# Performance work log

Hardware: AMD Instinct MI355X
Metric: run time of the kernel (lower is better)

## Reference

```python
import jax, jax.numpy as jnp
import numpy as np

N = 50000      # total nodes in batched graph
E = 800000     # total edges
G = 512        # number of graphs in the batch
NF = 32        # input node feature dim
EF = 16        # edge feature dim
HID = [64, 128, 128, 256]


def _seg_mean(vals, ids, num):
    s = jax.ops.segment_sum(vals, ids, num_segments=num)
    c = jax.ops.segment_sum(jnp.ones((vals.shape[0], 1), vals.dtype), ids, num_segments=num)
    return s / jnp.maximum(c, 1.0)


def setup_inputs() -> dict:
    key = jax.random.key(0)
    ks = list(jax.random.split(key, 64))
    it = iter(ks)

    def nk():
        return next(it)

    inp = {}
    inp["x"] = jax.random.normal(nk(), (N, NF), jnp.float32)
    inp["e"] = jax.random.normal(nk(), (E, EF), jnp.float32)
    inp["src"] = jax.random.randint(nk(), (E,), 0, N)
    inp["dst"] = jax.random.randint(nk(), (E,), 0, N)
    inp["gid"] = jnp.sort(jax.random.randint(nk(), (N,), 0, G))
    fin = NF
    for i, f in enumerate(HID):
        inp[f"Wm{i}"] = jax.random.normal(nk(), (fin + EF, f), jnp.float32) / np.sqrt(fin + EF)
        inp[f"bm{i}"] = jnp.zeros((f,), jnp.float32)
        inp[f"Ws{i}"] = jax.random.normal(nk(), (fin, f), jnp.float32) / np.sqrt(fin)
        inp[f"bs{i}"] = jnp.zeros((f,), jnp.float32)
        inp[f"Wc{i}"] = jax.random.normal(nk(), (f, 1), jnp.float32) / np.sqrt(f)
        inp[f"bc{i}"] = jnp.zeros((1,), jnp.float32)
        fin = f
    return inp


def _molconv(x, e, src, dst, Wm, bm, Ws, bs):
    # gather source node feats, condition on edge feats, per-edge MLP
    m = jax.nn.relu(jnp.concatenate([x[src], e], axis=-1) @ Wm + bm)  # [E, out]
    agg = _seg_mean(m, dst, x.shape[0])                               # scatter-mean to dst
    return jax.nn.relu(agg + x @ Ws + bs)                             # [N, out]


def reference(x, e, src, dst, gid,
              Wm0, bm0, Ws0, bs0, Wc0, bc0,
              Wm1, bm1, Ws1, bs1, Wc1, bc1,
              Wm2, bm2, Ws2, bs2, Wc2, bc2,
              Wm3, bm3, Ws3, bs3, Wc3, bc3):
    layers = [(Wm0, bm0, Ws0, bs0, Wc0, bc0),
              (Wm1, bm1, Ws1, bs1, Wc1, bc1),
              (Wm2, bm2, Ws2, bs2, Wc2, bc2),
              (Wm3, bm3, Ws3, bs3, Wc3, bc3)]
    feat = x
    score = jnp.zeros((G, 1), x.dtype)
    for Wm, bm, Ws, bs, Wc, bc in layers:
        feat = _molconv(feat, e, src, dst, Wm, bm, Ws, bs)
        # per-layer Linear(feats,1) classifier + AvgPooling per graph, summed
        score = score + _seg_mean(feat @ Wc + bc, gid, G)
    return score
```

## Files before the change

### kernel.cpp

```cpp
#include <hip/hip_runtime.h>

#define NN 50000
#define EE 800000
#define GG 512
#define NP 50048
#define EB 3125
#define SCB 196

typedef short bf16x8 __attribute__((ext_vector_type(8)));
typedef float floatx4 __attribute__((ext_vector_type(4)));

__device__ inline unsigned short f2b(float f) {
    unsigned u = __float_as_uint(f);
    unsigned r = (u + 0x7fffu + ((u >> 16) & 1u)) >> 16;
    return (unsigned short)r;
}
__device__ inline float b2f(unsigned short b) {
    return __uint_as_float(((unsigned)b) << 16);
}


__global__ void conv_all(const float* __restrict__ x, unsigned short* __restrict__ xb, long n8x,
                         const float* __restrict__ ef, unsigned short* __restrict__ efB, long n8e) {
    long i = (long)blockIdx.x * blockDim.x + threadIdx.x;
    const float* s;
    unsigned short* d;
    long idx;
    if (i < n8x) { s = x; d = xb; idx = i; }
    else if (i < n8x + n8e) { s = ef; d = efB; idx = i - n8x; }
    else return;
    float4 a = ((const float4*)s)[2 * idx];
    float4 b = ((const float4*)s)[2 * idx + 1];
    unsigned short o[8] = {f2b(a.x), f2b(a.y), f2b(a.z), f2b(a.w),
                           f2b(b.x), f2b(b.y), f2b(b.z), f2b(b.w)};
    ((uint4*)d)[idx] = *(uint4*)o;
}


struct TpD { const float* W; unsigned short* WT; int K, F, Kp, rowOff; };
struct TpTab { TpD d[12]; };

__global__ void tp_all(TpTab t) {
    TpD dd = t.d[blockIdx.y];
    int f = blockIdx.x;
    if (f >= dd.F) return;
    for (int k = threadIdx.x; k < dd.Kp; k += blockDim.x)
        dd.WT[(size_t)f * dd.Kp + k] =
            (k < dd.K) ? f2b(dd.W[(size_t)(dd.rowOff + k) * dd.F + f]) : (unsigned short)0;
}


__global__ void hist_cnt(const int* __restrict__ dst, int* __restrict__ hist,
                         const int* __restrict__ gid, float* __restrict__ gcnt) {
    int b = blockIdx.x;
    if (b < EB) {
        int e = b * 256 + threadIdx.x;
        if (e < EE) atomicAdd(&hist[dst[e]], 1);
    } else {
        int n = (b - EB) * 256 + threadIdx.x;
        if (n < NN) atomicAdd(&gcnt[gid[n]], 1.0f);
    }
}

__global__ void scanA(const int* __restrict__ hist, int* __restrict__ bsum) {
    __shared__ int sb[256];
    int idx = blockIdx.x * 256 + threadIdx.x;
    sb[threadIdx.x] = (idx < NN) ? hist[idx] : 0;
    __syncthreads();
    for (int off = 128; off > 0; off >>= 1) {
        if (threadIdx.x < off) sb[threadIdx.x] += sb[threadIdx.x + off];
        __syncthreads();
    }
    if (threadIdx.x == 0) bsum[blockIdx.x] = sb[0];
}

__global__ void scanB(const int* __restrict__ bsum, int* __restrict__ boff) {
    __shared__ int sb[256];
    int t = threadIdx.x;
    int v = (t < SCB) ? bsum[t] : 0;
    sb[t] = v;
    __syncthreads();
    for (int off = 1; off < 256; off <<= 1) {
        int u = (t >= off) ? sb[t - off] : 0;
        __syncthreads();
        sb[t] += u;
        __syncthreads();
    }
    if (t < SCB) boff[t] = sb[t] - v;
}

__global__ void scanC(const int* __restrict__ hist, const int* __restrict__ boff,
                      int* __restrict__ cursor, float* __restrict__ invdeg,
                      float* __restrict__ gcnt, float* __restrict__ score,
                      const float* __restrict__ bc0, const float* __restrict__ bc1,
                      const float* __restrict__ bc2, const float* __restrict__ bc3) {
    __shared__ int sb[256];
    int t = threadIdx.x;
    int idx = blockIdx.x * 256 + t;
    int v = (idx < NN) ? hist[idx] : 0;
    sb[t] = v;
    __syncthreads();
    for (int off = 1; off < 256; off <<= 1) {
        int u = (t >= off) ? sb[t - off] : 0;
        __syncthreads();
        sb[t] += u;
        __syncthreads();
    }
    if (idx < NN) {
        cursor[idx] = boff[blockIdx.x] + sb[t] - v;
        invdeg[idx] = 1.0f / fmaxf((float)v, 1.0f);
    }
    if (idx < GG) {
        float c = gcnt[idx];
        gcnt[idx] = 1.0f / fmaxf(c, 1.0f);
        score[idx] = (c > 0.0f) ? (bc0[0] + bc1[0] + bc2[0] + bc3[0]) : 0.0f;
    }
}

__global__ void scatter_kernel(const int* __restrict__ src, const int* __restrict__ dst,
                               int* __restrict__ cursor, const unsigned short* __restrict__ efB,
                               int* __restrict__ srcS, int* __restrict__ dstS,
                               unsigned short* __restrict__ efS) {
    int e = blockIdx.x * blockDim.x + threadIdx.x;
    if (e < EE) {
        int d = dst[e];
        int p = atomicAdd(&cursor[d], 1);
        srcS[p] = src[e];
        dstS[p] = d;
        const uint4* s = (const uint4*)&efB[(size_t)e * 16];
        uint4* dd = (uint4*)&efS[(size_t)p * 16];
        dd[0] = s[0];
        dd[1] = s[1];
    }
}


template<int FIN, int F>
__global__ __launch_bounds__(256)
void nodeP(const unsigned short* __restrict__ featB, const unsigned short* __restrict__ WxT,
           unsigned short* __restrict__ P)
{
    const int tid = threadIdx.x;
    const int w   = tid >> 6;
    const int l   = tid & 63;
    const int l16 = l & 15;
    const int q   = l >> 4;
    const int cb  = blockIdx.y * 64;
    const int nb  = blockIdx.x * 64;
    const int row = nb + w * 16 + l16;

    floatx4 acc[4];
    #pragma unroll
    for (int nt = 0; nt < 4; ++nt) acc[nt] = (floatx4){0.f, 0.f, 0.f, 0.f};

    #pragma unroll
    for (int kb = 0; kb < FIN; kb += 32) {
        bf16x8 a = *(const bf16x8*)&featB[(size_t)row * FIN + kb + q * 8];
        #pragma unroll
        for (int nt = 0; nt < 4; ++nt) {
            bf16x8 b = *(const bf16x8*)&WxT[(size_t)(cb + nt * 16 + l16) * FIN + kb + q * 8];
            acc[nt] = __builtin_amdgcn_mfma_f32_16x16x32_bf16(a, b, acc[nt], 0, 0, 0);
        }
    }

    #pragma unroll
    for (int nt = 0; nt < 4; ++nt)
        #pragma unroll
        for (int r = 0; r < 4; ++r) {
            int ro = nb + w * 16 + q * 4 + r;
            P[(size_t)ro * F + cb + nt * 16 + l16] = f2b(acc[nt][r]);
        }
}


template<int F>
__global__ __launch_bounds__(256)
void edge_q(const unsigned short* __restrict__ efS,
            const int* __restrict__ srcS, const int* __restrict__ dstS,
            const unsigned short* __restrict__ WeT, const unsigned short* __restrict__ P,
            const float* __restrict__ bm, float* __restrict__ agg)
{
    constexpr int CW  = (F >= 128) ? 128 : 64;
    constexpr int WPG = F / CW;
    constexpr int NT  = CW / 16;
    constexpr int EPB = 64 * (4 / WPG);
    constexpr int RS  = (CW == 128) ? 132 : 68;

    __shared__ __align__(16) float red[4][16 * RS];

    const int tid = threadIdx.x;
    const int w   = tid >> 6;
    const int l   = tid & 63;
    const int l16 = l & 15;
    const int q   = l >> 4;
    const int sub = w / WPG;
    const int cb  = (w % WPG) * CW;
    const int be  = blockIdx.x * EPB + sub * 64;

    const int dreg = dstS[be + l];
    const int sreg = srcS[be + l];

    const bf16x8 ZV = {0, 0, 0, 0, 0, 0, 0, 0};

    bf16x8 bfr[NT];
    #pragma unroll
    for (int nt = 0; nt < NT; ++nt)
        bfr[nt] = *(const bf16x8*)&WeT[(size_t)(cb + nt * 16 + l16) * 32 + q * 8];

    if constexpr (CW == 128) {
        float2 bmv;
        bmv.x = bm[cb + 2 * l];
        bmv.y = bm[cb + 2 * l + 1];

        int cur_d = -1;
        float2 csum = {0.f, 0.f};
        bool from_start = false;

        #pragma unroll
        for (int mt = 0; mt < 4; ++mt) {
            bf16x8 a = ZV;
            if (q < 2) a = *(const bf16x8*)&efS[(size_t)(be + mt * 16 + l16) * 16 + q * 8];
            floatx4 acc[NT];
            #pragma unroll
            for (int nt = 0; nt < NT; ++nt)
                acc[nt] = __builtin_amdgcn_mfma_f32_16x16x32_bf16(
                    a, bfr[nt], (floatx4){0.f, 0.f, 0.f, 0.f}, 0, 0, 0);

            unsigned pvv[16];
            #pragma unroll
            for (int r = 0; r < 16; ++r) {
                int sr = __shfl(sreg, mt * 16 + r);
                pvv[r] = *(const unsigned*)&P[(size_t)sr * F + cb + 2 * l];
            }

            #pragma unroll
            for (int nt = 0; nt < NT; ++nt)
                #pragma unroll
                for (int r4 = 0; r4 < 4; ++r4)
                    red[w][(q * 4 + r4) * RS + nt * 16 + l16] = acc[nt][r4];

            #pragma unroll
            for (int r = 0; r < 16; ++r) {
                int gr = mt * 16 + r;
                int d = __shfl(dreg, gr);
                float2 qv = *(const float2*)&red[w][r * RS + 2 * l];
                float2 v;
                v.x = fmaxf(qv.x + __uint_as_float(pvv[r] << 16)         + bmv.x, 0.f);
                v.y = fmaxf(qv.y + __uint_as_float(pvv[r] & 0xffff0000u) + bmv.y, 0.f);
                if (gr == 0) {
                    cur_d = d; csum = v; from_start = true;
                } else if (d != cur_d) {
                    float* ap = &agg[(size_t)cur_d * F + cb + 2 * l];
                    if (from_start) { atomicAdd(ap, csum.x); atomicAdd(ap + 1, csum.y); }
                    else            { *(float2*)ap = csum; }
                    cur_d = d; csum = v; from_start = false;
                } else {
                    csum.x += v.x; csum.y += v.y;
                }
            }
        }
        float* ap = &agg[(size_t)cur_d * F + cb + 2 * l];
        atomicAdd(ap, csum.x);
        atomicAdd(ap + 1, csum.y);
    } else {
        const float bmv = bm[cb + l];

        int cur_d = -1;
        float csum = 0.f;
        bool from_start = false;

        #pragma unroll
        for (int mt = 0; mt < 4; ++mt) {
            bf16x8 a = ZV;
            if (q < 2) a = *(const bf16x8*)&efS[(size_t)(be + mt * 16 + l16) * 16 + q * 8];
            floatx4 acc[NT];
            #pragma unroll
            for (int nt = 0; nt < NT; ++nt)
                acc[nt] = __builtin_amdgcn_mfma_f32_16x16x32_bf16(
                    a, bfr[nt], (floatx4){0.f, 0.f, 0.f, 0.f}, 0, 0, 0);

            float pv[16];
            #pragma unroll
            for (int r = 0; r < 16; ++r) {
                int sr = __shfl(sreg, mt * 16 + r);
                pv[r] = b2f(P[(size_t)sr * F + cb + l]);
            }

            #pragma unroll
            for (int nt = 0; nt < NT; ++nt)
                #pragma unroll
                for (int r4 = 0; r4 < 4; ++r4)
                    red[w][(q * 4 + r4) * RS + nt * 16 + l16] = acc[nt][r4];

            #pragma unroll
            for (int r = 0; r < 16; ++r) {
                int gr = mt * 16 + r;
                int d = __shfl(dreg, gr);
                float v = fmaxf(red[w][r * RS + l] + pv[r] + bmv, 0.f);
                if (gr == 0) {
                    cur_d = d; csum = v; from_start = true;
                } else if (d != cur_d) {
                    float* ap = &agg[(size_t)cur_d * F + cb + l];
                    if (from_start) atomicAdd(ap, csum);
                    else *ap = csum;
                    cur_d = d; csum = v; from_start = false;
                } else {
                    csum += v;
                }
            }
        }
        atomicAdd(&agg[(size_t)cur_d * F + cb + l], csum);
    }
}


template<int FIN, int F>
__global__ __launch_bounds__(256)
void node_mfma(const unsigned short* __restrict__ featB, const float* __restrict__ agg,
               const unsigned short* __restrict__ WsT, const float* __restrict__ bs,
               const float* __restrict__ Wc, const float* __restrict__ invdeg,
               unsigned short* __restrict__ fout, float* __restrict__ rd)
{
    const int tid = threadIdx.x;
    const int w   = tid >> 6;
    const int l   = tid & 63;
    const int l16 = l & 15;
    const int q   = l >> 4;
    const int cb  = blockIdx.y * 64;
    const int nb  = blockIdx.x * 64;
    const int row = nb + w * 16 + l16;

    floatx4 acc[4];
    #pragma unroll
    for (int nt = 0; nt < 4; ++nt) acc[nt] = (floatx4){0.f, 0.f, 0.f, 0.f};

    #pragma unroll
    for (int kb = 0; kb < FIN; kb += 32) {
        bf16x8 a = *(const bf16x8*)&featB[(size_t)row * FIN + kb + q * 8];
        #pragma unroll
        for (int nt = 0; nt < 4; ++nt) {
            bf16x8 b = *(const bf16x8*)&WsT[(size_t)(cb + nt * 16 + l16) * FIN + kb + q * 8];
            acc[nt] = __builtin_amdgcn_mfma_f32_16x16x32_bf16(a, b, acc[nt], 0, 0, 0);
        }
    }

    float wcv[4], bsv[4];
    #pragma unroll
    for (int nt = 0; nt < 4; ++nt) {
        wcv[nt] = Wc[cb + nt * 16 + l16];
        bsv[nt] = bs[cb + nt * 16 + l16];
    }

    #pragma unroll
    for (int r = 0; r < 4; ++r) {
        int n = nb + w * 16 + q * 4 + r;
        bool valid = n < NN;
        float idg = valid ? invdeg[n] : 0.f;
        float s = 0.f;
        #pragma unroll
        for (int nt = 0; nt < 4; ++nt) {
            int col = cb + nt * 16 + l16;
            float av = valid ? agg[(size_t)n * F + col] : 0.f;
            float v = fmaxf(acc[nt][r] + av * idg + bsv[nt], 0.f);
            if (valid) fout[(size_t)n * F + col] = f2b(v);
            s += v * wcv[nt];
        }
        s += __shfl_xor(s, 1);
        s += __shfl_xor(s, 2);
        s += __shfl_xor(s, 4);
        s += __shfl_xor(s, 8);
        if (valid && l16 == 0) atomicAdd(&rd[n], s);
    }
}


__global__ void score_reduce(const float* __restrict__ rd, const int* __restrict__ gid,
                             const float* __restrict__ invg, float* __restrict__ score) {
    int n = blockIdx.x * blockDim.x + threadIdx.x;
    int l = threadIdx.x & 63;
    bool valid = n < NN;
    int g = valid ? gid[n] : -1;
    float v = valid ? rd[n] : 0.f;
    #pragma unroll
    for (int off = 1; off < 64; off <<= 1) {
        float vo = __shfl_up(v, off);
        int go = __shfl_up(g, off);
        if (l >= off && go == g) v += vo;
    }
    int gn = __shfl_down(g, 1);
    bool tail = (l == 63) || (gn != g);
    if (valid && tail) atomicAdd(&score[g], v * invg[g]);
}


extern "C" void kernel_launch(void* const* d_in, const int* in_sizes, int n_in,
                              void* d_out, int out_size, void* d_ws, size_t ws_size,
                              hipStream_t stream) {
    const float* x   = (const float*)d_in[0];
    const float* ef  = (const float*)d_in[1];
    const int*   src = (const int*)d_in[2];
    const int*   dst = (const int*)d_in[3];
    const int*   gid = (const int*)d_in[4];
    const float *Wm[4], *bm[4], *Ws[4], *bs[4], *Wc[4], *bc[4];
    for (int i = 0; i < 4; ++i) {
        Wm[i] = (const float*)d_in[5 + 6 * i];
        bm[i] = (const float*)d_in[6 + 6 * i];
        Ws[i] = (const float*)d_in[7 + 6 * i];
        bs[i] = (const float*)d_in[8 + 6 * i];
        Wc[i] = (const float*)d_in[9 + 6 * i];
        bc[i] = (const float*)d_in[10 + 6 * i];
    }

    char* w = (char*)d_ws;
    float* agg = (float*)w;                  w += (size_t)NN * 256 * 4;
    unsigned short* xb  = (unsigned short*)w; w += (size_t)NP * 32 * 2;
    unsigned short* f1  = (unsigned short*)w; w += (size_t)NP * 64 * 2;
    unsigned short* f2  = (unsigned short*)w; w += (size_t)NP * 128 * 2;
    unsigned short* f3  = (unsigned short*)w; w += (size_t)NP * 128 * 2;
    unsigned short* f4  = (unsigned short*)w; w += (size_t)NP * 256 * 2;
    unsigned short* P   = (unsigned short*)w; w += (size_t)NP * 256 * 2;
    unsigned short* efB = (unsigned short*)w; w += (size_t)EE * 16 * 2;
    unsigned short* efS = (unsigned short*)w; w += (size_t)EE * 16 * 2;
    unsigned short* WxT0 = (unsigned short*)w; w += (size_t)64 * 32 * 2;
    unsigned short* WxT1 = (unsigned short*)w; w += (size_t)128 * 64 * 2;
    unsigned short* WxT2 = (unsigned short*)w; w += (size_t)128 * 128 * 2;
    unsigned short* WxT3 = (unsigned short*)w; w += (size_t)256 * 128 * 2;
    unsigned short* WeT0 = (unsigned short*)w; w += (size_t)64 * 32 * 2;
    unsigned short* WeT1 = (unsigned short*)w; w += (size_t)128 * 32 * 2;
    unsigned short* WeT2 = (unsigned short*)w; w += (size_t)128 * 32 * 2;
    unsigned short* WeT3 = (unsigned short*)w; w += (size_t)256 * 32 * 2;
    unsigned short* WsT0 = (unsigned short*)w; w += (size_t)64 * 32 * 2;
    unsigned short* WsT1 = (unsigned short*)w; w += (size_t)128 * 64 * 2;
    unsigned short* WsT2 = (unsigned short*)w; w += (size_t)128 * 128 * 2;
    unsigned short* WsT3 = (unsigned short*)w; w += (size_t)256 * 128 * 2;
    float* invdeg = (float*)w;               w += (size_t)NN * 4;
    float* invg   = (float*)w;               w += (size_t)GG * 4;
    float* rd     = (float*)w;               w += (size_t)NN * 4;
    int* hist   = (int*)w;                   w += (size_t)(NN + 1) * 4;
    int* srcS   = (int*)w;                   w += (size_t)EE * 4;
    int* dstS   = (int*)w;                   w += (size_t)EE * 4;
    int* bsum   = (int*)w;                   w += (size_t)SCB * 4;
    int* boff   = (int*)w;                   w += (size_t)SCB * 4;
    int* cursor = (int*)w;                   w += (size_t)NN * 4;
    float* score = (float*)d_out;

    const long n8x = (long)NN * 32 / 8, n8e = (long)EE * 16 / 8;
    conv_all<<<(n8x + n8e + 255) / 256, 256, 0, stream>>>(x, xb, n8x, ef, efB, n8e);

    TpTab tt;
    tt.d[0]  = {Wm[0], WxT0,  32,  64,  32,   0};
    tt.d[1]  = {Wm[1], WxT1,  64, 128,  64,   0};
    tt.d[2]  = {Wm[2], WxT2, 128, 128, 128,   0};
    tt.d[3]  = {Wm[3], WxT3, 128, 256, 128,   0};
    tt.d[4]  = {Wm[0], WeT0,  16,  64,  32,  32};
    tt.d[5]  = {Wm[1], WeT1,  16, 128,  32,  64};
    tt.d[6]  = {Wm[2], WeT2,  16, 128,  32, 128};
    tt.d[7]  = {Wm[3], WeT3,  16, 256,  32, 128};
    tt.d[8]  = {Ws[0], WsT0,  32,  64,  32,   0};
    tt.d[9]  = {Ws[1], WsT1,  64, 128,  64,   0};
    tt.d[10] = {Ws[2], WsT2, 128, 128, 128,   0};
    tt.d[11] = {Ws[3], WsT3, 128, 256, 128,   0};
    tp_all<<<dim3(256, 12), 256, 0, stream>>>(tt);

    hipMemsetAsync(invg, 0, (size_t)(GG + NN + NN + 1) * 4, stream);
    hist_cnt<<<EB + SCB, 256, 0, stream>>>(dst, hist, gid, invg);
    scanA<<<SCB, 256, 0, stream>>>(hist, bsum);
    scanB<<<1, 256, 0, stream>>>(bsum, boff);
    scanC<<<SCB, 256, 0, stream>>>(hist, boff, cursor, invdeg, invg, score,
                                   bc[0], bc[1], bc[2], bc[3]);
    scatter_kernel<<<EB, 256, 0, stream>>>(src, dst, cursor, efB, srcS, dstS, efS);

    const int NB = NP / 64;

    nodeP<32, 64><<<dim3(NB, 1), 256, 0, stream>>>(xb, WxT0, P);
    hipMemsetAsync(agg, 0, (size_t)NN * 64 * 4, stream);
    edge_q<64><<<EB, 256, 0, stream>>>(efS, srcS, dstS, WeT0, P, bm[0], agg);
    node_mfma<32, 64><<<dim3(NB, 1), 256, 0, stream>>>(xb, agg, WsT0, bs[0], Wc[0], invdeg, f1, rd);

    nodeP<64, 128><<<dim3(NB, 2), 256, 0, stream>>>(f1, WxT1, P);
    hipMemsetAsync(agg, 0, (size_t)NN * 128 * 4, stream);
    edge_q<128><<<EB, 256, 0, stream>>>(efS, srcS, dstS, WeT1, P, bm[1], agg);
    node_mfma<64, 128><<<dim3(NB, 2), 256, 0, stream>>>(f1, agg, WsT1, bs[1], Wc[1], invdeg, f2, rd);

    nodeP<128, 128><<<dim3(NB, 2), 256, 0, stream>>>(f2, WxT2, P);
    hipMemsetAsync(agg, 0, (size_t)NN * 128 * 4, stream);
    edge_q<128><<<EB, 256, 0, stream>>>(efS, srcS, dstS, WeT2, P, bm[2], agg);
    node_mfma<128, 128><<<dim3(NB, 2), 256, 0, stream>>>(f2, agg, WsT2, bs[2], Wc[2], invdeg, f3, rd);

    nodeP<128, 256><<<dim3(NB, 4), 256, 0, stream>>>(f3, WxT3, P);
    hipMemsetAsync(agg, 0, (size_t)NN * 256 * 4, stream);
    edge_q<256><<<EE / 128, 256, 0, stream>>>(efS, srcS, dstS, WeT3, P, bm[3], agg);
    node_mfma<128, 256><<<dim3(NB, 4), 256, 0, stream>>>(f3, agg, WsT3, bs[3], Wc[3], invdeg, f4, rd);

    score_reduce<<<SCB, 256, 0, stream>>>(rd, gid, invg, score);
}
```

Measured before the change: 710.9 us.

## Fuse agg zeroing into nodeP, prefetch edge tiles, swizzle LDS staging

The aggregation buffer is now zeroed inside the nodeP kernel instead of by a separate memset per layer, which saves a launch and one pass over memory. In edge_q, the edge-feature fragment and the gathered P values for the next 16-edge tile are loaded while the current tile is processed, so gather latency overlaps with compute. The LDS staging buffer drops its row padding and uses an XOR swizzle instead to avoid bank conflicts. In exchange, the double-buffered arrays raise register pressure.

```diff
diff --git a/kernel.cpp b/kernel.cpp
--- a/kernel.cpp
+++ b/kernel.cpp
@@ -138,7 +138,7 @@
 template<int FIN, int F>
 __global__ __launch_bounds__(256)
 void nodeP(const unsigned short* __restrict__ featB, const unsigned short* __restrict__ WxT,
-           unsigned short* __restrict__ P)
+           unsigned short* __restrict__ P, float* __restrict__ agg)
 {
     const int tid = threadIdx.x;
     const int w   = tid >> 6;
@@ -148,6 +148,17 @@
     const int cb  = blockIdx.y * 64;
     const int nb  = blockIdx.x * 64;
     const int row = nb + w * 16 + l16;
+
+    {
+        const int zr = nb + (tid >> 4);
+        const int zc = cb + ((tid & 15) << 2);
+        const float4 z4 = {0.f, 0.f, 0.f, 0.f};
+        #pragma unroll
+        for (int i = 0; i < 4; ++i) {
+            int n = zr + i * 16;
+            if (n < NN) *(float4*)&agg[(size_t)n * F + zc] = z4;
+        }
+    }
 
     floatx4 acc[4];
     #pragma unroll
@@ -184,7 +195,7 @@
     constexpr int WPG = F / CW;
     constexpr int NT  = CW / 16;
     constexpr int EPB = 64 * (4 / WPG);
-    constexpr int RS  = (CW == 128) ? 132 : 68;
+    constexpr int RS  = CW;
 
     __shared__ __align__(16) float red[4][16 * RS];
 
@@ -201,6 +212,8 @@
     const int sreg = srcS[be + l];
 
     const bf16x8 ZV = {0, 0, 0, 0, 0, 0, 0, 0};
+    const int xo = q << 3;
+    float* redw = &red[w][0];
 
     bf16x8 bfr[NT];
     #pragma unroll
@@ -216,36 +229,43 @@
         float2 csum = {0.f, 0.f};
         bool from_start = false;
 
+        bf16x8 a_cur = ZV, a_nxt;
+        if (q < 2) a_cur = *(const bf16x8*)&efS[(size_t)(be + l16) * 16 + q * 8];
+        unsigned pvv[16], pvn[16];
+        #pragma unroll
+        for (int r = 0; r < 16; ++r) {
+            int sr = __shfl(sreg, r);
+            pvv[r] = *(const unsigned*)&P[(size_t)sr * F + cb + 2 * l];
+        }
+
         #pragma unroll
         for (int mt = 0; mt < 4; ++mt) {
-            bf16x8 a = ZV;
-            if (q < 2) a = *(const bf16x8*)&efS[(size_t)(be + mt * 16 + l16) * 16 + q * 8];
-            floatx4 acc[NT];
+            if (mt < 3) {
+                a_nxt = ZV;
+                if (q < 2) a_nxt = *(const bf16x8*)&efS[(size_t)(be + (mt + 1) * 16 + l16) * 16 + q * 8];
+            }
             #pragma unroll
-            for (int nt = 0; nt < NT; ++nt)
-                acc[nt] = __builtin_amdgcn_mfma_f32_16x16x32_bf16(
-                    a, bfr[nt], (floatx4){0.f, 0.f, 0.f, 0.f}, 0, 0, 0);
-
-            unsigned pvv[16];
-            #pragma unroll
-            for (int r = 0; r < 16; ++r) {
-                int sr = __shfl(sreg, mt * 16 + r);
-                pvv[r] = *(const unsigned*)&P[(size_t)sr * F + cb + 2 * l];
-            }
-
-            #pragma unroll
-            for (int nt = 0; nt < NT; ++nt)
+            for (int nt = 0; nt < NT; ++nt) {
+                floatx4 acc = __builtin_amdgcn_mfma_f32_16x16x32_bf16(
+                    a_cur, bfr[nt], (floatx4){0.f, 0.f, 0.f, 0.f}, 0, 0, 0);
                 #pragma unroll
                 for (int r4 = 0; r4 < 4; ++r4)
-                    red[w][(q * 4 + r4) * RS + nt * 16 + l16] = acc[nt][r4];
-
+                    redw[(q * 4 + r4) * RS + ((nt * 16 + l16) ^ xo)] = acc[r4];
+            }
+            if (mt < 3) {
+                #pragma unroll
+                for (int r = 0; r < 16; ++r) {
+                    int sr = __shfl(sreg, (mt + 1) * 16 + r);
+                    pvn[r] = *(const unsigned*)&P[(size_t)sr * F + cb + 2 * l];
+                }
+            }
             #pragma unroll
             for (int r = 0; r < 16; ++r) {
                 int gr = mt * 16 + r;
                 int d = __shfl(dreg, gr);
-                float2 qv = *(const float2*)&red[w][r * RS + 2 * l];
+                float2 qv = *(const float2*)&redw[r * RS + ((2 * l) ^ (((r >> 2) & 3) << 3))];
                 float2 v;
-                v.x = fmaxf(qv.x + __uint_as_float(pvv[r] << 16)         + bmv.x, 0.f);
+                v.x = fmaxf(qv.x + __uint_as_float(pvv[r] << 16)          + bmv.x, 0.f);
                 v.y = fmaxf(qv.y + __uint_as_float(pvv[r] & 0xffff0000u) + bmv.y, 0.f);
                 if (gr == 0) {
                     cur_d = d; csum = v; from_start = true;
@@ -258,6 +278,11 @@
                     csum.x += v.x; csum.y += v.y;
                 }
             }
+            if (mt < 3) {
+                #pragma unroll
+                for (int r = 0; r < 16; ++r) pvv[r] = pvn[r];
+                a_cur = a_nxt;
+            }
         }
         float* ap = &agg[(size_t)cur_d * F + cb + 2 * l];
         atomicAdd(ap, csum.x);
@@ -269,34 +294,42 @@
         float csum = 0.f;
         bool from_start = false;
 
+        bf16x8 a_cur = ZV, a_nxt;
+        if (q < 2) a_cur = *(const bf16x8*)&efS[(size_t)(be + l16) * 16 + q * 8];
+        float pvv[16], pvn[16];
+        #pragma unroll
+        for (int r = 0; r < 16; ++r) {
+            int sr = __shfl(sreg, r);
+            pvv[r] = b2f(P[(size_t)sr * F + cb + l]);
+        }
+
         #pragma unroll
         for (int mt = 0; mt < 4; ++mt) {
-            bf16x8 a = ZV;
-            if (q < 2) a = *(const bf16x8*)&efS[(size_t)(be + mt * 16 + l16) * 16 + q * 8];
-            floatx4 acc[NT];
+            if (mt < 3) {
+                a_nxt = ZV;
+                if (q < 2) a_nxt = *(const bf16x8*)&efS[(size_t)(be + (mt + 1) * 16 + l16) * 16 + q * 8];
+            }
             #pragma unroll
-            for (int nt = 0; nt < NT; ++nt)
-                acc[nt] = __builtin_amdgcn_mfma_f32_16x16x32_bf16(
-                    a, bfr[nt], (floatx4){0.f, 0.f, 0.f, 0.f}, 0, 0, 0);
-
-            float pv[16];
-            #pragma unroll
-            for (int r = 0; r < 16; ++r) {
-                int sr = __shfl(sreg, mt * 16 + r);
-                pv[r] = b2f(P[(size_t)sr * F + cb + l]);
-            }
-
-            #pragma unroll
-            for (int nt = 0; nt < NT; ++nt)
+            for (int nt = 0; nt < NT; ++nt) {
+                floatx4 acc = __builtin_amdgcn_mfma_f32_16x16x32_bf16(
+                    a_cur, bfr[nt], (floatx4){0.f, 0.f, 0.f, 0.f}, 0, 0, 0);
                 #pragma unroll
                 for (int r4 = 0; r4 < 4; ++r4)
-                    red[w][(q * 4 + r4) * RS + nt * 16 + l16] = acc[nt][r4];
-
+                    redw[(q * 4 + r4) * RS + ((nt * 16 + l16) ^ xo)] = acc[r4];
+            }
+            if (mt < 3) {
+                #pragma unroll
+                for (int r = 0; r < 16; ++r) {
+                    int sr = __shfl(sreg, (mt + 1) * 16 + r);
+                    pvn[r] = b2f(P[(size_t)sr * F + cb + l]);
+                }
+            }
             #pragma unroll
             for (int r = 0; r < 16; ++r) {
                 int gr = mt * 16 + r;
                 int d = __shfl(dreg, gr);
-                float v = fmaxf(red[w][r * RS + l] + pv[r] + bmv, 0.f);
+                float qv = redw[r * RS + (l ^ (((r >> 2) & 3) << 3))];
+                float v = fmaxf(qv + pvv[r] + bmv, 0.f);
                 if (gr == 0) {
                     cur_d = d; csum = v; from_start = true;
                 } else if (d != cur_d) {
@@ -307,6 +340,11 @@
                 } else {
                     csum += v;
                 }
+            }
+            if (mt < 3) {
+                #pragma unroll
+                for (int r = 0; r < 16; ++r) pvv[r] = pvn[r];
+                a_cur = a_nxt;
             }
         }
         atomicAdd(&agg[(size_t)cur_d * F + cb + l], csum);
@@ -472,23 +510,19 @@
 
     const int NB = NP / 64;
 
-    nodeP<32, 64><<<dim3(NB, 1), 256, 0, stream>>>(xb, WxT0, P);
-    hipMemsetAsync(agg, 0, (size_t)NN * 64 * 4, stream);
+    nodeP<32, 64><<<dim3(NB, 1), 256, 0, stream>>>(xb, WxT0, P, agg);
     edge_q<64><<<EB, 256, 0, stream>>>(efS, srcS, dstS, WeT0, P, bm[0], agg);
     node_mfma<32, 64><<<dim3(NB, 1), 256, 0, stream>>>(xb, agg, WsT0, bs[0], Wc[0], invdeg, f1, rd);
 
-    nodeP<64, 128><<<dim3(NB, 2), 256, 0, stream>>>(f1, WxT1, P);
-    hipMemsetAsync(agg, 0, (size_t)NN * 128 * 4, stream);
+    nodeP<64, 128><<<dim3(NB, 2), 256, 0, stream>>>(f1, WxT1, P, agg);
     edge_q<128><<<EB, 256, 0, stream>>>(efS, srcS, dstS, WeT1, P, bm[1], agg);
     node_mfma<64, 128><<<dim3(NB, 2), 256, 0, stream>>>(f1, agg, WsT1, bs[1], Wc[1], invdeg, f2, rd);
 
-    nodeP<128, 128><<<dim3(NB, 2), 256, 0, stream>>>(f2, WxT2, P);
-    hipMemsetAsync(agg, 0, (size_t)NN * 128 * 4, stream);
+    nodeP<128, 128><<<dim3(NB, 2), 256, 0, stream>>>(f2, WxT2, P, agg);
     edge_q<128><<<EB, 256, 0, stream>>>(efS, srcS, dstS, WeT2, P, bm[2], agg);
     node_mfma<128, 128><<<dim3(NB, 2), 256, 0, stream>>>(f2, agg, WsT2, bs[2], Wc[2], invdeg, f3, rd);
 
-    nodeP<128, 256><<<dim3(NB, 4), 256, 0, stream>>>(f3, WxT3, P);
-    hipMemsetAsync(agg, 0, (size_t)NN * 256 * 4, stream);
+    nodeP<128, 256><<<dim3(NB, 4), 256, 0, stream>>>(f3, WxT3, P, agg);
     edge_q<256><<<EE / 128, 256, 0, stream>>>(efS, srcS, dstS, WeT3, P, bm[3], agg);
     node_mfma<128, 256><<<dim3(NB, 4), 256, 0, stream>>>(f3, agg, WsT3, bs[3], Wc[3], invdeg, f4, rd);
 
```

New measurement: 686.4 us. 3.4% less time.

## Double-buffer edge gathers into LDS, fuse agg zeroing into nodeP

Applied to the files above, without the earlier changes.

The edge kernel now gathers source-node projections and edge features straight into per-wave LDS buffers with asynchronous global-to-LDS loads. It double-buffers them so the next 16-edge tile loads while the current one computes. The column width per wave is fixed at 64 for every layer, so wider layers use more blocks. LDS writes use XOR swizzling to avoid bank conflicts. The separate memset of the aggregation buffer is folded into the nodeP kernel, which removes extra launches and a full write pass, at the cost of hand-written waitcnt bookkeeping.

```diff
diff --git a/kernel.cpp b/kernel.cpp
--- a/kernel.cpp
+++ b/kernel.cpp
@@ -18,6 +18,13 @@
 __device__ inline float b2f(unsigned short b) {
     return __uint_as_float(((unsigned)b) << 16);
 }
+
+#define GLD16(gp, lp) __builtin_amdgcn_global_load_lds( \
+    (const __attribute__((address_space(1))) void*)(gp), \
+    (__attribute__((address_space(3))) void*)(lp), 16, 0, 0)
+#define GLD4(gp, lp) __builtin_amdgcn_global_load_lds( \
+    (const __attribute__((address_space(1))) void*)(gp), \
+    (__attribute__((address_space(3))) void*)(lp), 4, 0, 0)
 
 
 __global__ void conv_all(const float* __restrict__ x, unsigned short* __restrict__ xb, long n8x,
@@ -138,7 +145,7 @@
 template<int FIN, int F>
 __global__ __launch_bounds__(256)
 void nodeP(const unsigned short* __restrict__ featB, const unsigned short* __restrict__ WxT,
-           unsigned short* __restrict__ P)
+           unsigned short* __restrict__ P, float* __restrict__ agg)
 {
     const int tid = threadIdx.x;
     const int w   = tid >> 6;
@@ -149,6 +156,17 @@
     const int nb  = blockIdx.x * 64;
     const int row = nb + w * 16 + l16;
 
+    {
+        const int zr = nb + (tid >> 4);
+        const int zc = cb + ((tid & 15) << 2);
+        const float4 z4 = {0.f, 0.f, 0.f, 0.f};
+        #pragma unroll
+        for (int i = 0; i < 4; ++i) {
+            int n = zr + i * 16;
+            if (n < NN) *(float4*)&agg[(size_t)n * F + zc] = z4;
+        }
+    }
+
     floatx4 acc[4];
     #pragma unroll
     for (int nt = 0; nt < 4; ++nt) acc[nt] = (floatx4){0.f, 0.f, 0.f, 0.f};
@@ -172,6 +190,8 @@
         }
 }
 
+
+#define RXO(r) ((((r) >> 2 & 1) << 4) | (((r) >> 3 & 1) << 3))
 
 template<int F>
 __global__ __launch_bounds__(256)
@@ -180,13 +200,15 @@
             const unsigned short* __restrict__ WeT, const unsigned short* __restrict__ P,
             const float* __restrict__ bm, float* __restrict__ agg)
 {
-    constexpr int CW  = (F >= 128) ? 128 : 64;
+    constexpr int CW  = 64;
     constexpr int WPG = F / CW;
-    constexpr int NT  = CW / 16;
+    constexpr int NT  = 4;
     constexpr int EPB = 64 * (4 / WPG);
-    constexpr int RS  = (CW == 128) ? 132 : 68;
+    constexpr int RS  = 64;
 
     __shared__ __align__(16) float red[4][16 * RS];
+    __shared__ __align__(16) unsigned short stgP[4][2][16 * 64];
+    __shared__ __align__(16) unsigned short stgE[4][2][16 * 16];
 
     const int tid = threadIdx.x;
     const int w   = tid >> 6;
@@ -200,117 +222,82 @@
     const int dreg = dstS[be + l];
     const int sreg = srcS[be + l];
 
+    const int grow = l >> 3;
+    const int gchk = l & 7;
+
     const bf16x8 ZV = {0, 0, 0, 0, 0, 0, 0, 0};
+    const int xo = ((q & 1) << 4) | ((q >> 1) << 3);
+    float* redw = &red[w][0];
 
     bf16x8 bfr[NT];
     #pragma unroll
     for (int nt = 0; nt < NT; ++nt)
         bfr[nt] = *(const bf16x8*)&WeT[(size_t)(cb + nt * 16 + l16) * 32 + q * 8];
 
-    if constexpr (CW == 128) {
-        float2 bmv;
-        bmv.x = bm[cb + 2 * l];
-        bmv.y = bm[cb + 2 * l + 1];
-
-        int cur_d = -1;
-        float2 csum = {0.f, 0.f};
-        bool from_start = false;
-
-        #pragma unroll
-        for (int mt = 0; mt < 4; ++mt) {
-            bf16x8 a = ZV;
-            if (q < 2) a = *(const bf16x8*)&efS[(size_t)(be + mt * 16 + l16) * 16 + q * 8];
-            floatx4 acc[NT];
+    const float bmv = bm[cb + l];
+
+    {
+        int sr0 = __shfl(sreg, grow);
+        int sr1 = __shfl(sreg, 8 + grow);
+        GLD16(&P[(size_t)sr0 * F + cb + gchk * 8], &stgP[w][0][0]);
+        GLD16(&P[(size_t)sr1 * F + cb + gchk * 8], &stgP[w][0][512]);
+        GLD4(&efS[(size_t)(be + grow) * 16 + gchk * 2],      &stgE[w][0][0]);
+        GLD4(&efS[(size_t)(be + 8 + grow) * 16 + gchk * 2],  &stgE[w][0][128]);
+    }
+
+    int cur_d = -1;
+    float csum = 0.f;
+    bool from_start = false;
+
+    #pragma unroll
+    for (int mt = 0; mt < 4; ++mt) {
+        const int bufc = mt & 1;
+        if (mt < 3) {
+            int sr0 = __shfl(sreg, (mt + 1) * 16 + grow);
+            int sr1 = __shfl(sreg, (mt + 1) * 16 + 8 + grow);
+            GLD16(&P[(size_t)sr0 * F + cb + gchk * 8], &stgP[w][bufc ^ 1][0]);
+            GLD16(&P[(size_t)sr1 * F + cb + gchk * 8], &stgP[w][bufc ^ 1][512]);
+            GLD4(&efS[(size_t)(be + (mt + 1) * 16 + grow) * 16 + gchk * 2],
+                 &stgE[w][bufc ^ 1][0]);
+            GLD4(&efS[(size_t)(be + (mt + 1) * 16 + 8 + grow) * 16 + gchk * 2],
+                 &stgE[w][bufc ^ 1][128]);
+        }
+        if (mt < 3) asm volatile("s_waitcnt vmcnt(4)" ::: "memory");
+        else        asm volatile("s_waitcnt vmcnt(0)" ::: "memory");
+        __builtin_amdgcn_sched_barrier(0);
+
+        bf16x8 a = ZV;
+        if (q < 2) a = *(const bf16x8*)&stgE[w][bufc][l16 * 16 + q * 8];
+
+        #pragma unroll
+        for (int nt = 0; nt < NT; ++nt) {
+            floatx4 acc = __builtin_amdgcn_mfma_f32_16x16x32_bf16(
+                a, bfr[nt], (floatx4){0.f, 0.f, 0.f, 0.f}, 0, 0, 0);
             #pragma unroll
-            for (int nt = 0; nt < NT; ++nt)
-                acc[nt] = __builtin_amdgcn_mfma_f32_16x16x32_bf16(
-                    a, bfr[nt], (floatx4){0.f, 0.f, 0.f, 0.f}, 0, 0, 0);
-
-            unsigned pvv[16];
-            #pragma unroll
-            for (int r = 0; r < 16; ++r) {
-                int sr = __shfl(sreg, mt * 16 + r);
-                pvv[r] = *(const unsigned*)&P[(size_t)sr * F + cb + 2 * l];
+            for (int r4 = 0; r4 < 4; ++r4)
+                redw[(q * 4 + r4) * RS + ((nt * 16 + l16) ^ xo)] = acc[r4];
+        }
+
+        const unsigned short* stw = &stgP[w][bufc][0];
+        #pragma unroll
+        for (int r = 0; r < 16; ++r) {
+            int gr = mt * 16 + r;
+            int d = __shfl(dreg, gr);
+            float qv = redw[r * RS + (l ^ RXO(r))];
+            float v = fmaxf(qv + b2f(stw[r * 64 + l]) + bmv, 0.f);
+            if (gr == 0) {
+                cur_d = d; csum = v; from_start = true;
+            } else if (d != cur_d) {
+                float* ap = &agg[(size_t)cur_d * F + cb + l];
+                if (from_start) atomicAdd(ap, csum);
+                else *ap = csum;
+                cur_d = d; csum = v; from_start = false;
+            } else {
+                csum += v;
             }
-
-            #pragma unroll
-            for (int nt = 0; nt < NT; ++nt)
-                #pragma unroll
-                for (int r4 = 0; r4 < 4; ++r4)
-                    red[w][(q * 4 + r4) * RS + nt * 16 + l16] = acc[nt][r4];
-
-            #pragma unroll
-            for (int r = 0; r < 16; ++r) {
-                int gr = mt * 16 + r;
-                int d = __shfl(dreg, gr);
-                float2 qv = *(const float2*)&red[w][r * RS + 2 * l];
-                float2 v;
-                v.x = fmaxf(qv.x + __uint_as_float(pvv[r] << 16)         + bmv.x, 0.f);
-                v.y = fmaxf(qv.y + __uint_as_float(pvv[r] & 0xffff0000u) + bmv.y, 0.f);
-                if (gr == 0) {
-                    cur_d = d; csum = v; from_start = true;
-                } else if (d != cur_d) {
-                    float* ap = &agg[(size_t)cur_d * F + cb + 2 * l];
-                    if (from_start) { atomicAdd(ap, csum.x); atomicAdd(ap + 1, csum.y); }
-                    else            { *(float2*)ap = csum; }
-                    cur_d = d; csum = v; from_start = false;
-                } else {
-                    csum.x += v.x; csum.y += v.y;
-                }
-            }
-        }
-        float* ap = &agg[(size_t)cur_d * F + cb + 2 * l];
-        atomicAdd(ap, csum.x);
-        atomicAdd(ap + 1, csum.y);
-    } else {
-        const float bmv = bm[cb + l];
-
-        int cur_d = -1;
-        float csum = 0.f;
-        bool from_start = false;
-
-        #pragma unroll
-        for (int mt = 0; mt < 4; ++mt) {
-            bf16x8 a = ZV;
-            if (q < 2) a = *(const bf16x8*)&efS[(size_t)(be + mt * 16 + l16) * 16 + q * 8];
-            floatx4 acc[NT];
-            #pragma unroll
-            for (int nt = 0; nt < NT; ++nt)
-                acc[nt] = __builtin_amdgcn_mfma_f32_16x16x32_bf16(
-                    a, bfr[nt], (floatx4){0.f, 0.f, 0.f, 0.f}, 0, 0, 0);
-
-            float pv[16];
-            #pragma unroll
-            for (int r = 0; r < 16; ++r) {
-                int sr = __shfl(sreg, mt * 16 + r);
-                pv[r] = b2f(P[(size_t)sr * F + cb + l]);
-            }
-
-            #pragma unroll
-            for (int nt = 0; nt < NT; ++nt)
-                #pragma unroll
-                for (int r4 = 0; r4 < 4; ++r4)
-                    red[w][(q * 4 + r4) * RS + nt * 16 + l16] = acc[nt][r4];
-
-            #pragma unroll
-            for (int r = 0; r < 16; ++r) {
-                int gr = mt * 16 + r;
-                int d = __shfl(dreg, gr);
-                float v = fmaxf(red[w][r * RS + l] + pv[r] + bmv, 0.f);
-                if (gr == 0) {
-                    cur_d = d; csum = v; from_start = true;
-                } else if (d != cur_d) {
-                    float* ap = &agg[(size_t)cur_d * F + cb + l];
-                    if (from_start) atomicAdd(ap, csum);
-                    else *ap = csum;
-                    cur_d = d; csum = v; from_start = false;
-                } else {
-                    csum += v;
-                }
-            }
-        }
-        atomicAdd(&agg[(size_t)cur_d * F + cb + l], csum);
-    }
+        }
+    }
+    atomicAdd(&agg[(size_t)cur_d * F + cb + l], csum);
 }
 
 
@@ -472,24 +459,20 @@
 
     const int NB = NP / 64;
 
-    nodeP<32, 64><<<dim3(NB, 1), 256, 0, stream>>>(xb, WxT0, P);
-    hipMemsetAsync(agg, 0, (size_t)NN * 64 * 4, stream);
+    nodeP<32, 64><<<dim3(NB, 1), 256, 0, stream>>>(xb, WxT0, P, agg);
     edge_q<64><<<EB, 256, 0, stream>>>(efS, srcS, dstS, WeT0, P, bm[0], agg);
     node_mfma<32, 64><<<dim3(NB, 1), 256, 0, stream>>>(xb, agg, WsT0, bs[0], Wc[0], invdeg, f1, rd);
 
-    nodeP<64, 128><<<dim3(NB, 2), 256, 0, stream>>>(f1, WxT1, P);
-    hipMemsetAsync(agg, 0, (size_t)NN * 128 * 4, stream);
-    edge_q<128><<<EB, 256, 0, stream>>>(efS, srcS, dstS, WeT1, P, bm[1], agg);
+    nodeP<64, 128><<<dim3(NB, 2), 256, 0, stream>>>(f1, WxT1, P, agg);
+    edge_q<128><<<EE / 128, 256, 0, stream>>>(efS, srcS, dstS, WeT1, P, bm[1], agg);
     node_mfma<64, 128><<<dim3(NB, 2), 256, 0, stream>>>(f1, agg, WsT1, bs[1], Wc[1], invdeg, f2, rd);
 
-    nodeP<128, 128><<<dim3(NB, 2), 256, 0, stream>>>(f2, WxT2, P);
-    hipMemsetAsync(agg, 0, (size_t)NN * 128 * 4, stream);
-    edge_q<128><<<EB, 256, 0, stream>>>(efS, srcS, dstS, WeT2, P, bm[2], agg);
+    nodeP<128, 128><<<dim3(NB, 2), 256, 0, stream>>>(f2, WxT2, P, agg);
+    edge_q<128><<<EE / 128, 256, 0, stream>>>(efS, srcS, dstS, WeT2, P, bm[2], agg);
     node_mfma<128, 128><<<dim3(NB, 2), 256, 0, stream>>>(f2, agg, WsT2, bs[2], Wc[2], invdeg, f3, rd);
 
-    nodeP<128, 256><<<dim3(NB, 4), 256, 0, stream>>>(f3, WxT3, P);
-    hipMemsetAsync(agg, 0, (size_t)NN * 256 * 4, stream);
-    edge_q<256><<<EE / 128, 256, 0, stream>>>(efS, srcS, dstS, WeT3, P, bm[3], agg);
+    nodeP<128, 256><<<dim3(NB, 4), 256, 0, stream>>>(f3, WxT3, P, agg);
+    edge_q<256><<<EE / 64, 256, 0, stream>>>(efS, srcS, dstS, WeT3, P, bm[3], agg);
     node_mfma<128, 256><<<dim3(NB, 4), 256, 0, stream>>>(f3, agg, WsT3, bs[3], Wc[3], invdeg, f4, rd);
 
     score_reduce<<<SCB, 256, 0, stream>>>(rd, gid, invg, score);
```

After: 749.3 us. 5.4% more time.

## Fuse agg zeroing into nodeP, ballot segment ends, XOR-swizzle LDS reduction

Applied to the files above, without the earlier changes.

Zeroes the aggregation buffer inside the nodeP kernel, so the four separate memset launches go away. In edge_q, segment boundaries are precomputed with a wave ballot over neighbouring dst values, which replaces the per-row cur_d compare/shuffle chain. The LDS staging buffer drops its padding and uses an XOR swizzle to avoid bank conflicts. MFMA results are now produced and stored per tile, which cuts live accumulator registers. The risk is that the swizzle and boundary logic (first/last segment atomics) must exactly match the old semantics.

```diff
diff --git a/kernel.cpp b/kernel.cpp
--- a/kernel.cpp
+++ b/kernel.cpp
@@ -138,7 +138,7 @@
 template<int FIN, int F>
 __global__ __launch_bounds__(256)
 void nodeP(const unsigned short* __restrict__ featB, const unsigned short* __restrict__ WxT,
-           unsigned short* __restrict__ P)
+           unsigned short* __restrict__ P, float* __restrict__ agg)
 {
     const int tid = threadIdx.x;
     const int w   = tid >> 6;
@@ -149,6 +149,17 @@
     const int nb  = blockIdx.x * 64;
     const int row = nb + w * 16 + l16;
 
+    {
+        const int zr = nb + (tid >> 4);
+        const int zc = cb + ((tid & 15) << 2);
+        const float4 z4 = {0.f, 0.f, 0.f, 0.f};
+        #pragma unroll
+        for (int i = 0; i < 4; ++i) {
+            int n = zr + i * 16;
+            if (n < NN) *(float4*)&agg[(size_t)n * F + zc] = z4;
+        }
+    }
+
     floatx4 acc[4];
     #pragma unroll
     for (int nt = 0; nt < 4; ++nt) acc[nt] = (floatx4){0.f, 0.f, 0.f, 0.f};
@@ -172,6 +183,8 @@
         }
 }
 
+
+#define RXO(r) ((((r) >> 2 & 1) << 4) | (((r) >> 3 & 1) << 3))
 
 template<int F>
 __global__ __launch_bounds__(256)
@@ -184,7 +197,7 @@
     constexpr int WPG = F / CW;
     constexpr int NT  = CW / 16;
     constexpr int EPB = 64 * (4 / WPG);
-    constexpr int RS  = (CW == 128) ? 132 : 68;
+    constexpr int RS  = CW;
 
     __shared__ __align__(16) float red[4][16 * RS];
 
@@ -200,7 +213,12 @@
     const int dreg = dstS[be + l];
     const int sreg = srcS[be + l];
 
+    const int dnext = __shfl_down(dreg, 1);
+    const unsigned long long em = __ballot((l == 63) || (dreg != dnext));
+
     const bf16x8 ZV = {0, 0, 0, 0, 0, 0, 0, 0};
+    const int xo = ((q & 1) << 4) | ((q >> 1) << 3);
+    float* redw = &red[w][0];
 
     bf16x8 bfr[NT];
     #pragma unroll
@@ -212,20 +230,13 @@
         bmv.x = bm[cb + 2 * l];
         bmv.y = bm[cb + 2 * l + 1];
 
-        int cur_d = -1;
         float2 csum = {0.f, 0.f};
-        bool from_start = false;
+        bool first = true;
 
         #pragma unroll
         for (int mt = 0; mt < 4; ++mt) {
             bf16x8 a = ZV;
             if (q < 2) a = *(const bf16x8*)&efS[(size_t)(be + mt * 16 + l16) * 16 + q * 8];
-            floatx4 acc[NT];
-            #pragma unroll
-            for (int nt = 0; nt < NT; ++nt)
-                acc[nt] = __builtin_amdgcn_mfma_f32_16x16x32_bf16(
-                    a, bfr[nt], (floatx4){0.f, 0.f, 0.f, 0.f}, 0, 0, 0);
-
             unsigned pvv[16];
             #pragma unroll
             for (int r = 0; r < 16; ++r) {
@@ -234,82 +245,71 @@
             }
 
             #pragma unroll
-            for (int nt = 0; nt < NT; ++nt)
+            for (int nt = 0; nt < NT; ++nt) {
+                floatx4 acc = __builtin_amdgcn_mfma_f32_16x16x32_bf16(
+                    a, bfr[nt], (floatx4){0.f, 0.f, 0.f, 0.f}, 0, 0, 0);
                 #pragma unroll
                 for (int r4 = 0; r4 < 4; ++r4)
-                    red[w][(q * 4 + r4) * RS + nt * 16 + l16] = acc[nt][r4];
+                    redw[(q * 4 + r4) * RS + ((nt * 16 + l16) ^ xo)] = acc[r4];
+            }
 
             #pragma unroll
             for (int r = 0; r < 16; ++r) {
-                int gr = mt * 16 + r;
-                int d = __shfl(dreg, gr);
-                float2 qv = *(const float2*)&red[w][r * RS + 2 * l];
-                float2 v;
-                v.x = fmaxf(qv.x + __uint_as_float(pvv[r] << 16)         + bmv.x, 0.f);
-                v.y = fmaxf(qv.y + __uint_as_float(pvv[r] & 0xffff0000u) + bmv.y, 0.f);
-                if (gr == 0) {
-                    cur_d = d; csum = v; from_start = true;
-                } else if (d != cur_d) {
-                    float* ap = &agg[(size_t)cur_d * F + cb + 2 * l];
-                    if (from_start) { atomicAdd(ap, csum.x); atomicAdd(ap + 1, csum.y); }
-                    else            { *(float2*)ap = csum; }
-                    cur_d = d; csum = v; from_start = false;
-                } else {
-                    csum.x += v.x; csum.y += v.y;
+                const int gr = mt * 16 + r;
+                float2 qv = *(const float2*)&redw[r * RS + ((2 * l) ^ RXO(r))];
+                csum.x += fmaxf(qv.x + __uint_as_float(pvv[r] << 16)          + bmv.x, 0.f);
+                csum.y += fmaxf(qv.y + __uint_as_float(pvv[r] & 0xffff0000u) + bmv.y, 0.f);
+                if ((em >> gr) & 1ull) {
+                    int d = __shfl(dreg, gr);
+                    float* ap = &agg[(size_t)d * F + cb + 2 * l];
+                    if (first || gr == 63) { atomicAdd(ap, csum.x); atomicAdd(ap + 1, csum.y); }
+                    else                   { *(float2*)ap = csum; }
+                    csum.x = 0.f; csum.y = 0.f;
+                    first = false;
                 }
             }
         }
-        float* ap = &agg[(size_t)cur_d * F + cb + 2 * l];
-        atomicAdd(ap, csum.x);
-        atomicAdd(ap + 1, csum.y);
     } else {
         const float bmv = bm[cb + l];
 
-        int cur_d = -1;
         float csum = 0.f;
-        bool from_start = false;
+        bool first = true;
 
         #pragma unroll
         for (int mt = 0; mt < 4; ++mt) {
             bf16x8 a = ZV;
             if (q < 2) a = *(const bf16x8*)&efS[(size_t)(be + mt * 16 + l16) * 16 + q * 8];
-            floatx4 acc[NT];
-            #pragma unroll
-            for (int nt = 0; nt < NT; ++nt)
-                acc[nt] = __builtin_amdgcn_mfma_f32_16x16x32_bf16(
-                    a, bfr[nt], (floatx4){0.f, 0.f, 0.f, 0.f}, 0, 0, 0);
-
-            float pv[16];
+            float pvv[16];
             #pragma unroll
             for (int r = 0; r < 16; ++r) {
                 int sr = __shfl(sreg, mt * 16 + r);
-                pv[r] = b2f(P[(size_t)sr * F + cb + l]);
-            }
-
-            #pragma unroll
-            for (int nt = 0; nt < NT; ++nt)
+                pvv[r] = b2f(P[(size_t)sr * F + cb + l]);
+            }
+
+            #pragma unroll
+            for (int nt = 0; nt < NT; ++nt) {
+                floatx4 acc = __builtin_amdgcn_mfma_f32_16x16x32_bf16(
+                    a, bfr[nt], (floatx4){0.f, 0.f, 0.f, 0.f}, 0, 0, 0);
                 #pragma unroll
                 for (int r4 = 0; r4 < 4; ++r4)
-                    red[w][(q * 4 + r4) * RS + nt * 16 + l16] = acc[nt][r4];
+                    redw[(q * 4 + r4) * RS + ((nt * 16 + l16) ^ xo)] = acc[r4];
+            }
 
             #pragma unroll
             for (int r = 0; r < 16; ++r) {
-                int gr = mt * 16 + r;
-                int d = __shfl(dreg, gr);
-                float v = fmaxf(red[w][r * RS + l] + pv[r] + bmv, 0.f);
-                if (gr == 0) {
-                    cur_d = d; csum = v; from_start = true;
-                } else if (d != cur_d) {
-                    float* ap = &agg[(size_t)cur_d * F + cb + l];
-                    if (from_start) atomicAdd(ap, csum);
-                    else *ap = csum;
-                    cur_d = d; csum = v; from_start = false;
-                } else {
-                    csum += v;
+                const int gr = mt * 16 + r;
+                float qv = redw[r * RS + (l ^ RXO(r))];
+                csum += fmaxf(qv + pvv[r] + bmv, 0.f);
+                if ((em >> gr) & 1ull) {
+                    int d = __shfl(dreg, gr);
+                    float* ap = &agg[(size_t)d * F + cb + l];
+                    if (first || gr == 63) atomicAdd(ap, csum);
+                    else                   *ap = csum;
+                    csum = 0.f;
+                    first = false;
                 }
             }
         }
-        atomicAdd(&agg[(size_t)cur_d * F + cb + l], csum);
     }
 }
 
@@ -472,23 +472,19 @@
 
     const int NB = NP / 64;
 
-    nodeP<32, 64><<<dim3(NB, 1), 256, 0, stream>>>(xb, WxT0, P);
-    hipMemsetAsync(agg, 0, (size_t)NN * 64 * 4, stream);
+    nodeP<32, 64><<<dim3(NB, 1), 256, 0, stream>>>(xb, WxT0, P, agg);
     edge_q<64><<<EB, 256, 0, stream>>>(efS, srcS, dstS, WeT0, P, bm[0], agg);
     node_mfma<32, 64><<<dim3(NB, 1), 256, 0, stream>>>(xb, agg, WsT0, bs[0], Wc[0], invdeg, f1, rd);
 
-    nodeP<64, 128><<<dim3(NB, 2), 256, 0, stream>>>(f1, WxT1, P);
-    hipMemsetAsync(agg, 0, (size_t)NN * 128 * 4, stream);
+    nodeP<64, 128><<<dim3(NB, 2), 256, 0, stream>>>(f1, WxT1, P, agg);
     edge_q<128><<<EB, 256, 0, stream>>>(efS, srcS, dstS, WeT1, P, bm[1], agg);
     node_mfma<64, 128><<<dim3(NB, 2), 256, 0, stream>>>(f1, agg, WsT1, bs[1], Wc[1], invdeg, f2, rd);
 
-    nodeP<128, 128><<<dim3(NB, 2), 256, 0, stream>>>(f2, WxT2, P);
-    hipMemsetAsync(agg, 0, (size_t)NN * 128 * 4, stream);
+    nodeP<128, 128><<<dim3(NB, 2), 256, 0, stream>>>(f2, WxT2, P, agg);
     edge_q<128><<<EB, 256, 0, stream>>>(efS, srcS, dstS, WeT2, P, bm[2], agg);
     node_mfma<128, 128><<<dim3(NB, 2), 256, 0, stream>>>(f2, agg, WsT2, bs[2], Wc[2], invdeg, f3, rd);
 
-    nodeP<128, 256><<<dim3(NB, 4), 256, 0, stream>>>(f3, WxT3, P);
-    hipMemsetAsync(agg, 0, (size_t)NN * 256 * 4, stream);
+    nodeP<128, 256><<<dim3(NB, 4), 256, 0, stream>>>(f3, WxT3, P, agg);
     edge_q<256><<<EE / 128, 256, 0, stream>>>(efS, srcS, dstS, WeT3, P, bm[3], agg);
     node_mfma<128, 256><<<dim3(NB, 4), 256, 0, stream>>>(f3, agg, WsT3, bs[3], Wc[3], invdeg, f4, rd);
 
```

Result: faster. 665.5 us (-6.4%).
